# Kernel tuning notes

Hardware: AMD Instinct MI355X
Metric: run time of the kernel (lower is better)

The kernel has to match this reference:

```python
import jax, jax.numpy as jnp
import numpy as np

TOPK = 8
EPS = 1e-12  # matches torch F.normalize default eps


def setup_inputs() -> dict:
    key = jax.random.key(0)
    x = jax.random.normal(key, (8, 2048, 128), dtype=jnp.float32)
    return {"x": x}


def reference(x) -> jnp.ndarray:
    B, N, D = x.shape
    # --- pairwise dot scores on L2-normalized features (cosine similarity) ---
    norm = jnp.sqrt(jnp.sum(x * x, axis=-1, keepdims=True))
    normed = x / jnp.maximum(norm, EPS)
    scores = jnp.einsum('bnd,bmd->bnm', normed, normed)  # [B, N, N]

    # --- top-k per row -> binary adjacency via scatter ---
    _, idx = jax.lax.top_k(scores, TOPK)  # [B, N, k]
    bi = jnp.arange(B)[:, None, None]
    ni = jnp.arange(N)[None, :, None]
    adj = jnp.zeros((B, N, N), dtype=x.dtype).at[bi, ni, idx].set(1.0)

    # --- symmetrize and add self loops ---
    adj = jnp.maximum(adj, jnp.swapaxes(adj, 1, 2))
    eye = jnp.eye(N, dtype=x.dtype)
    adj = jnp.maximum(adj, eye[None, :, :])
    return adj
```

## Files before the change

kernel.cpp:

```cpp
#include <hip/hip_runtime.h>
#include <cstdint>

#define NN 2048
#define DD 128
#define BATCH 8
#define NROWS 16384
#define MARGIN 0.02f
#define CAP2 48

typedef __attribute__((ext_vector_type(8))) short bf16x8;
typedef __attribute__((ext_vector_type(4))) float f32x4;
typedef unsigned long long u64;
typedef unsigned int u32;
typedef unsigned short u16;

__device__ __forceinline__ u32 bf16rne(float f) {
  u32 u = __float_as_uint(f);
  return (u + 0x7fffu + ((u >> 16) & 1u)) >> 16;
}

__global__ __launch_bounds__(256) void k_normalize(const float* __restrict__ x,
                                                   double* __restrict__ rinv,
                                                   u32* __restrict__ nb,
                                                   float4* __restrict__ outz) {
  const int wave = threadIdx.x >> 6, lane = threadIdx.x & 63;
  const long long row = (long long)blockIdx.x * 4 + wave;
  float2 v = ((const float2*)(x + row * DD))[lane];
  const double d0 = v.x, d1 = v.y;
  double s = d0 * d0 + d1 * d1;
  #pragma unroll
  for (int m = 32; m >= 1; m >>= 1) s += __shfl_xor(s, m, 64);
  double den = sqrt(s); den = den > 1e-12 ? den : 1e-12;
  if (lane == 0) rinv[row] = 1.0 / den;
  double2 o; o.x = d0 / den; o.y = d1 / den;
  nb[row * (DD / 2) + lane] = bf16rne((float)o.x) | (bf16rne((float)o.y) << 16);

  {
    const int base = blockIdx.x * 256 + threadIdx.x;
    const float4 zf = {0.0f, 0.0f, 0.0f, 0.0f};
    #pragma unroll
    for (int k = 0; k < 8; ++k) outz[base + k * 1048576] = zf;
  }
}

#define CXF(i, j) { const float a_ = L[i], b_ = L[j]; L[i] = fmaxf(a_, b_); L[j] = fminf(a_, b_); }
__device__ __forceinline__ void merge8f(float (&kv)[8], const float (&ov)[8]) {
  float L[8];
  #pragma unroll
  for (int i = 0; i < 8; ++i) L[i] = fmaxf(kv[i], ov[7 - i]);
  CXF(0, 4) CXF(1, 5) CXF(2, 6) CXF(3, 7)
  CXF(0, 2) CXF(1, 3) CXF(4, 6) CXF(5, 7)
  CXF(0, 1) CXF(2, 3) CXF(4, 5) CXF(6, 7)
  #pragma unroll
  for (int i = 0; i < 8; ++i) kv[i] = L[i];
}

__device__ __forceinline__ u64 make_key(double s, int col) {
  u64 u = (u64)__double_as_longlong(s);
  const u64 m = (u64)((long long)u >> 63);
  u ^= (m | 0x8000000000000000ull);
  return (u & ~2047ull) | (u64)(2047 - col);
}
__device__ __forceinline__ u64 umax64(u64 a, u64 b) { return a > b ? a : b; }
__device__ __forceinline__ u64 umin64(u64 a, u64 b) { return a > b ? b : a; }
__device__ __forceinline__ void merge8(u64 (&kv)[8], const u64 (&ov)[8]) {
  u64 L[8];
  #pragma unroll
  for (int i = 0; i < 8; ++i) L[i] = umax64(kv[i], ov[7 - i]);
#define CX(i, j) { const u64 a_ = L[i], b_ = L[j]; L[i] = umax64(a_, b_); L[j] = umin64(a_, b_); }
  CX(0, 4) CX(1, 5) CX(2, 6) CX(3, 7)
  CX(0, 2) CX(1, 3) CX(4, 6) CX(5, 7)
  CX(0, 1) CX(2, 3) CX(4, 5) CX(6, 7)
#undef CX
  #pragma unroll
  for (int i = 0; i < 8; ++i) kv[i] = L[i];
}
__device__ __forceinline__ void insert8u(u64 (&v)[8], u64 nk) {
  if (nk > v[7]) {
    v[7] = nk;
    #pragma unroll
    for (int q = 7; q >= 1; --q) {
      const u64 a = v[q - 1], b = v[q];
      const bool sw = b > a;
      v[q - 1] = sw ? b : a; v[q] = sw ? a : b;
    }
  }
}

__global__ __launch_bounds__(1024) void k_build(const u32* __restrict__ nb,
                                                const float* __restrict__ x,
                                                const double* __restrict__ rinv,
                                                float* __restrict__ out) {
  __shared__ float bmf[64][130];
  __shared__ float thl[64];
  __shared__ u32 cnt[64];
  __shared__ u32 cand[64][CAP2];

  const int tid = threadIdx.x; const int w = tid >> 6; const int l = tid & 63;
  const int q = l >> 4; const int m = l & 15;
  const int rowblk = blockIdx.x;
  const int row0 = rowblk * 64;
  const int b = rowblk >> 5;
  const long long brow = (long long)b * NN;

  bf16x8 pvals = {0,0,0,0,0,0,0,0}, pones = {0,0,0,0,0,0,0,0};
  if (q == 0) {
    pvals[0] = (short)(__float_as_uint((float)(m + 1)) >> 16);
    pones[0] = (short)(__float_as_uint(1.0f) >> 16);
  }
  const f32x4 z4 = {0.0f, 0.0f, 0.0f, 0.0f};
  const f32x4 pr  = __builtin_amdgcn_mfma_f32_16x16x32_bf16(pvals, pones, z4, 0, 0, 0);
  const f32x4 pr2 = __builtin_amdgcn_mfma_f32_16x16x32_bf16(pones, pvals, z4, 0, 0, 0);
  int cof[4];
  #pragma unroll
  for (int p = 0; p < 4; ++p) cof[p] = (int)pr[p] - 1;
  const int rof = (int)pr2[0] - 1;

  if (tid < 64) cnt[tid] = 0u;

  bf16x8 ar4[4][4];
  #pragma unroll
  for (int rf = 0; rf < 4; ++rf) {
    const u32* Ap = nb + (long long)(row0 + 16 * rf + m) * (DD / 2) + 4 * q;
    #pragma unroll
    for (int cc = 0; cc < 4; ++cc) ar4[rf][cc] = *(const bf16x8*)(Ap + 16 * cc);
  }

  const int c0w = w * 128;
  const u32* Bb = nb + (brow + c0w) * (DD / 2);
  bf16x8 bcA[4], bcB[4];

#define LOADB(DST, T) { const u32* p_ = Bb + (long long)(16 * (T) + m) * (DD / 2) + 4 * q; \
  _Pragma("unroll") for (int cc = 0; cc < 4; ++cc) DST[cc] = *(const bf16x8*)(p_ + 16 * cc); }

#define TILE1(BC, T) {                                                             \
    _Pragma("unroll") for (int rf = 0; rf < 4; ++rf) {                             \
      f32x4 acc = z4;                                                              \
      _Pragma("unroll") for (int cc = 0; cc < 4; ++cc)                             \
        acc = __builtin_amdgcn_mfma_f32_16x16x32_bf16(BC[cc], ar4[rf][cc], acc, 0, 0, 0); \
      float bm_ = fmaxf(fmaxf(acc[0], acc[1]), fmaxf(acc[2], acc[3]));             \
      bm_ = fmaxf(bm_, __shfl_xor(bm_, 16, 64));                                   \
      bm_ = fmaxf(bm_, __shfl_xor(bm_, 32, 64));                                   \
      if (q == 0) bmf[16 * rf + m][w * 8 + (T)] = bm_;                             \
    } }

  LOADB(bcA, 0)
  #pragma unroll
  for (int t = 0; t < 8; t += 2) {
    LOADB(bcB, t + 1)
    TILE1(bcA, t)
    if (t + 2 < 8) LOADB(bcA, t + 2)
    TILE1(bcB, t + 1)
  }
#undef TILE1
  __syncthreads();

  for (int j = 0; j < 4; ++j) {
    const int rib = w * 4 + j;
    const float b0 = bmf[rib][2 * l];
    const float b1 = bmf[rib][2 * l + 1];
    float mx = fmaxf(b0, b1);
    float kv8[8];
    {
      const float o  = __shfl_xor(mx, 1, 64);
      const float h2 = fmaxf(mx, o), l2 = fminf(mx, o);
      const float p0 = __shfl_xor(h2, 2, 64), p1 = __shfl_xor(l2, 2, 64);
      const float m0 = fmaxf(h2, p0);
      const float xx = fminf(h2, p0);
      const float yy = fmaxf(l2, p1);
      const float m3 = fminf(l2, p1);
      const float m1 = fmaxf(xx, yy);
      const float m2 = fminf(xx, yy);
      const float q0 = __shfl_xor(m0, 4, 64), q1 = __shfl_xor(m1, 4, 64);
      const float q2 = __shfl_xor(m2, 4, 64), q3 = __shfl_xor(m3, 4, 64);
      float L[8] = {m0, m1, m2, m3, q3, q2, q1, q0};
      CXF(0, 4) CXF(1, 5) CXF(2, 6) CXF(3, 7)
      CXF(0, 2) CXF(1, 3) CXF(4, 6) CXF(5, 7)
      CXF(0, 1) CXF(2, 3) CXF(4, 5) CXF(6, 7)
      #pragma unroll
      for (int s = 0; s < 8; ++s) kv8[s] = L[s];
      #pragma unroll
      for (int mk = 8; mk <= 32; mk <<= 1) {
        float ov[8];
        #pragma unroll
        for (int s = 0; s < 8; ++s) ov[s] = __shfl_xor(kv8[s], mk, 64);
        merge8f(kv8, ov);
      }
    }
    if (l == 0) thl[rib] = kv8[7] - MARGIN;
  }
  __syncthreads();

  float th4[4]; int rib4[4];
  #pragma unroll
  for (int rf = 0; rf < 4; ++rf) {
    rib4[rf] = 16 * rf + rof;
    th4[rf] = thl[rib4[rf]];
  }

#define TILEF(BC, T) {                                                             \
    _Pragma("unroll") for (int rf = 0; rf < 4; ++rf) {                             \
      f32x4 acc = z4;                                                              \
      _Pragma("unroll") for (int cc = 0; cc < 4; ++cc)                             \
        acc = __builtin_amdgcn_mfma_f32_16x16x32_bf16(BC[cc], ar4[rf][cc], acc, 0, 0, 0); \
      _Pragma("unroll") for (int p = 0; p < 4; ++p) {                              \
        if (acc[p] >= th4[rf]) {                                                   \
          const u32 id = atomicAdd(&cnt[rib4[rf]], 1u);                            \
          if (id < CAP2) cand[rib4[rf]][id] = (u32)(c0w + 16 * (T) + cof[p]);      \
        }                                                                          \
      }                                                                            \
    } }

  LOADB(bcA, 0)
  #pragma unroll
  for (int t = 0; t < 8; t += 2) {
    LOADB(bcB, t + 1)
    TILEF(bcA, t)
    if (t + 2 < 8) LOADB(bcA, t + 2)
    TILEF(bcB, t + 1)
  }
#undef TILEF
#undef LOADB
  __syncthreads();

  for (int j = 0; j < 4; ++j) {
    const int rib = w * 4 + j;
    const int r = row0 + rib;
    const int n = r & (NN - 1);
    const int c = (int)cnt[rib];
    const double ri = rinv[r];
    u64 kv[8];
    #pragma unroll
    for (int s = 0; s < 8; ++s) kv[s] = 0ull;

    if (c <= CAP2) {
      float2 a4[4];
      #pragma unroll
      for (int jj = 0; jj < 4; ++jj)
        a4[jj] = ((const float2*)(x + (long long)r * DD))[m + 16 * jj];

      for (int i = 0; i < c; i += 4) {
        const int gi = i + q;
        const bool valid = gi < c;
        const int col = valid ? (int)cand[rib][gi] : 0;
        const float2* cp = (const float2*)(x + (brow + col) * DD);
        double d = 0.0;
        #pragma unroll
        for (int jj = 0; jj < 4; ++jj) {
          const float2 bv = cp[m + 16 * jj];
          d = fma((double)a4[jj].x, (double)bv.x, d);
          d = fma((double)a4[jj].y, (double)bv.y, d);
        }
        #pragma unroll
        for (int mk = 1; mk <= 8; mk <<= 1) d += __shfl_xor(d, mk, 64);
        if (valid) insert8u(kv, make_key(d * ri * rinv[brow + col], col));
      }
      #pragma unroll
      for (int mk = 16; mk <= 32; mk <<= 1) {
        u64 ov[8];
        #pragma unroll
        for (int s = 0; s < 8; ++s) ov[s] = __shfl_xor(kv[s], mk, 64);
        merge8(kv, ov);
      }
    } else {
      for (int base = 0; base < NN; base += 64) {
        const int col = base + l;
        const float* ap = x + (long long)r * DD;
        const float* cp2 = x + (brow + col) * DD;
        double d = 0.0;
        for (int kk = 0; kk < 64; ++kk) {
          const float2 av = ((const float2*)ap)[kk];
          const float2 bv = ((const float2*)cp2)[kk];
          d = fma((double)av.x, (double)bv.x, fma((double)av.y, (double)bv.y, d));
        }
        d = d * ri * rinv[brow + col];
        u64 one[8];
        one[0] = make_key(d, col);
        #pragma unroll
        for (int s = 1; s < 8; ++s) one[s] = 0ull;
        #pragma unroll
        for (int mk = 1; mk <= 32; mk <<= 1) {
          u64 ov[8];
          #pragma unroll
          for (int s = 0; s < 8; ++s) ov[s] = __shfl_xor(one[s], mk, 64);
          merge8(one, ov);
        }
        merge8(kv, one);
      }
    }

    const long long orow = (long long)r * NN;
    const long long obase = brow * NN;
    if (l == 8) out[orow + n] = 1.0f;
    #pragma unroll
    for (int s = 0; s < 8; ++s) {
      const int mcol = 2047 - (int)(kv[s] & 2047ull);
      if (l == s) {
        out[orow + mcol] = 1.0f;
        out[obase + (long long)mcol * NN + n] = 1.0f;
      }
    }
  }
}

extern "C" void kernel_launch(void* const* d_in, const int* in_sizes, int n_in,
                              void* d_out, int out_size, void* d_ws, size_t ws_size,
                              hipStream_t stream) {
  const float* x = (const float*)d_in[0];
  float* out = (float*)d_out;
  char* ws = (char*)d_ws;
  u32* nb = (u32*)ws;
  double* rinv = (double*)(ws + 4194304);

  hipLaunchKernelGGL(k_normalize, dim3(NROWS / 4), dim3(256), 0, stream, x, rinv, nb,
                     (float4*)out);
  hipLaunchKernelGGL(k_build, dim3(256), dim3(1024), 0, stream, nb, x, rinv, out);
}
```

Before: 228.6 us.

## Cache bf16-rounded scores in registers instead of recomputing the GEMM pass

The build kernel used to compute the score tiles twice: once to get per-tile maxima for a threshold, and again to collect candidates. It now runs a single MFMA pass and keeps the scores in registers, packed as bf16 values rounded upward so the threshold filter stays conservative. Blocks are retiled to 32 rows with 512 threads, each wave covering 256 columns, and the candidate capacity is raised to 64. This removes half of the MFMA work and the repeated B loads, at the cost of about 64 extra VGPRs per thread and possibly more candidates per row, since the rounded values are coarser.

Result: slower. 250.7 us (+9.7%).

```diff
diff --git a/kernel.cpp b/kernel.cpp
--- a/kernel.cpp
+++ b/kernel.cpp
@@ -6,7 +6,7 @@
 #define BATCH 8
 #define NROWS 16384
 #define MARGIN 0.02f
-#define CAP2 48
+#define CAP2 64
 
 typedef __attribute__((ext_vector_type(8))) short bf16x8;
 typedef __attribute__((ext_vector_type(4))) float f32x4;
@@ -17,6 +17,10 @@
 __device__ __forceinline__ u32 bf16rne(float f) {
   u32 u = __float_as_uint(f);
   return (u + 0x7fffu + ((u >> 16) & 1u)) >> 16;
+}
+__device__ __forceinline__ u32 bf16up(float f) {
+  const u32 u = __float_as_uint(f);
+  return (u + (((int)u >= 0) ? 0xFFFFu : 0u)) >> 16;
 }
 
 __global__ __launch_bounds__(256) void k_normalize(const float* __restrict__ x,
@@ -87,20 +91,19 @@
   }
 }
 
-__global__ __launch_bounds__(1024) void k_build(const u32* __restrict__ nb,
-                                                const float* __restrict__ x,
-                                                const double* __restrict__ rinv,
-                                                float* __restrict__ out) {
-  __shared__ float bmf[64][130];
-  __shared__ float thl[64];
-  __shared__ u32 cnt[64];
-  __shared__ u32 cand[64][CAP2];
+__global__ __launch_bounds__(512, 4) void k_build(const u32* __restrict__ nb,
+                                                  const float* __restrict__ x,
+                                                  const double* __restrict__ rinv,
+                                                  float* __restrict__ out) {
+  __shared__ float bmf[32][130];
+  __shared__ float thl[32];
+  __shared__ u32 cnt[32];
+  __shared__ u32 cand[32][CAP2];
 
   const int tid = threadIdx.x; const int w = tid >> 6; const int l = tid & 63;
   const int q = l >> 4; const int m = l & 15;
-  const int rowblk = blockIdx.x;
-  const int row0 = rowblk * 64;
-  const int b = rowblk >> 5;
+  const int row0 = blockIdx.x * 32;
+  const int b = blockIdx.x >> 6;
   const long long brow = (long long)b * NN;
 
   bf16x8 pvals = {0,0,0,0,0,0,0,0}, pones = {0,0,0,0,0,0,0,0};
@@ -116,43 +119,40 @@
   for (int p = 0; p < 4; ++p) cof[p] = (int)pr[p] - 1;
   const int rof = (int)pr2[0] - 1;
 
-  if (tid < 64) cnt[tid] = 0u;
-
-  bf16x8 ar4[4][4];
-  #pragma unroll
-  for (int rf = 0; rf < 4; ++rf) {
+  if (tid < 32) cnt[tid] = 0u;
+
+  bf16x8 ar4[2][4];
+  #pragma unroll
+  for (int rf = 0; rf < 2; ++rf) {
     const u32* Ap = nb + (long long)(row0 + 16 * rf + m) * (DD / 2) + 4 * q;
     #pragma unroll
     for (int cc = 0; cc < 4; ++cc) ar4[rf][cc] = *(const bf16x8*)(Ap + 16 * cc);
   }
 
-  const int c0w = w * 128;
+  const int c0w = w * 256;
   const u32* Bb = nb + (brow + c0w) * (DD / 2);
-  bf16x8 bcA[4], bcB[4];
-
-#define LOADB(DST, T) { const u32* p_ = Bb + (long long)(16 * (T) + m) * (DD / 2) + 4 * q; \
-  _Pragma("unroll") for (int cc = 0; cc < 4; ++cc) DST[cc] = *(const bf16x8*)(p_ + 16 * cc); }
-
-#define TILE1(BC, T) {                                                             \
-    _Pragma("unroll") for (int rf = 0; rf < 4; ++rf) {                             \
-      f32x4 acc = z4;                                                              \
-      _Pragma("unroll") for (int cc = 0; cc < 4; ++cc)                             \
-        acc = __builtin_amdgcn_mfma_f32_16x16x32_bf16(BC[cc], ar4[rf][cc], acc, 0, 0, 0); \
-      float bm_ = fmaxf(fmaxf(acc[0], acc[1]), fmaxf(acc[2], acc[3]));             \
-      bm_ = fmaxf(bm_, __shfl_xor(bm_, 16, 64));                                   \
-      bm_ = fmaxf(bm_, __shfl_xor(bm_, 32, 64));                                   \
-      if (q == 0) bmf[16 * rf + m][w * 8 + (T)] = bm_;                             \
-    } }
-
-  LOADB(bcA, 0)
-  #pragma unroll
-  for (int t = 0; t < 8; t += 2) {
-    LOADB(bcB, t + 1)
-    TILE1(bcA, t)
-    if (t + 2 < 8) LOADB(bcA, t + 2)
-    TILE1(bcB, t + 1)
-  }
-#undef TILE1
+  bf16x8 bc[4];
+  uint2 pk[32];
+
+  #pragma unroll
+  for (int t = 0; t < 16; ++t) {
+    { const u32* p_ = Bb + (long long)(16 * t + m) * (DD / 2) + 4 * q;
+      #pragma unroll
+      for (int cc = 0; cc < 4; ++cc) bc[cc] = *(const bf16x8*)(p_ + 16 * cc); }
+    #pragma unroll
+    for (int rf = 0; rf < 2; ++rf) {
+      f32x4 acc = z4;
+      #pragma unroll
+      for (int cc = 0; cc < 4; ++cc)
+        acc = __builtin_amdgcn_mfma_f32_16x16x32_bf16(bc[cc], ar4[rf][cc], acc, 0, 0, 0);
+      float bm_ = fmaxf(fmaxf(acc[0], acc[1]), fmaxf(acc[2], acc[3]));
+      bm_ = fmaxf(bm_, __shfl_xor(bm_, 16, 64));
+      bm_ = fmaxf(bm_, __shfl_xor(bm_, 32, 64));
+      if (q == 0) bmf[16 * rf + m][w * 16 + t] = bm_;
+      pk[t * 2 + rf].x = bf16up(acc[0]) | (bf16up(acc[1]) << 16);
+      pk[t * 2 + rf].y = bf16up(acc[2]) | (bf16up(acc[3]) << 16);
+    }
+  }
   __syncthreads();
 
   for (int j = 0; j < 4; ++j) {
@@ -191,36 +191,32 @@
   }
   __syncthreads();
 
-  float th4[4]; int rib4[4];
-  #pragma unroll
-  for (int rf = 0; rf < 4; ++rf) {
-    rib4[rf] = 16 * rf + rof;
-    th4[rf] = thl[rib4[rf]];
-  }
-
-#define TILEF(BC, T) {                                                             \
-    _Pragma("unroll") for (int rf = 0; rf < 4; ++rf) {                             \
-      f32x4 acc = z4;                                                              \
-      _Pragma("unroll") for (int cc = 0; cc < 4; ++cc)                             \
-        acc = __builtin_amdgcn_mfma_f32_16x16x32_bf16(BC[cc], ar4[rf][cc], acc, 0, 0, 0); \
-      _Pragma("unroll") for (int p = 0; p < 4; ++p) {                              \
-        if (acc[p] >= th4[rf]) {                                                   \
-          const u32 id = atomicAdd(&cnt[rib4[rf]], 1u);                            \
-          if (id < CAP2) cand[rib4[rf]][id] = (u32)(c0w + 16 * (T) + cof[p]);      \
-        }                                                                          \
-      }                                                                            \
-    } }
-
-  LOADB(bcA, 0)
-  #pragma unroll
-  for (int t = 0; t < 8; t += 2) {
-    LOADB(bcB, t + 1)
-    TILEF(bcA, t)
-    if (t + 2 < 8) LOADB(bcA, t + 2)
-    TILEF(bcB, t + 1)
-  }
-#undef TILEF
-#undef LOADB
+  {
+    float th2[2]; int rib2[2];
+    #pragma unroll
+    for (int rf = 0; rf < 2; ++rf) {
+      rib2[rf] = 16 * rf + rof;
+      th2[rf] = thl[rib2[rf]];
+    }
+    #pragma unroll
+    for (int t = 0; t < 16; ++t)
+      #pragma unroll
+      for (int rf = 0; rf < 2; ++rf) {
+        const uint2 pv = pk[t * 2 + rf];
+        float v0 = __uint_as_float(pv.x << 16);
+        float v1 = __uint_as_float(pv.x & 0xFFFF0000u);
+        float v2 = __uint_as_float(pv.y << 16);
+        float v3 = __uint_as_float(pv.y & 0xFFFF0000u);
+        #pragma unroll
+        for (int p = 0; p < 4; ++p) {
+          const float vv = (p == 0) ? v0 : (p == 1) ? v1 : (p == 2) ? v2 : v3;
+          if (vv >= th2[rf]) {
+            const u32 id = atomicAdd(&cnt[rib2[rf]], 1u);
+            if (id < CAP2) cand[rib2[rf]][id] = (u32)(c0w + 16 * t + cof[p]);
+          }
+        }
+      }
+  }
   __syncthreads();
 
   for (int j = 0; j < 4; ++j) {
@@ -314,5 +310,5 @@
 
   hipLaunchKernelGGL(k_normalize, dim3(NROWS / 4), dim3(256), 0, stream, x, rinv, nb,
                      (float4*)out);
-  hipLaunchKernelGGL(k_build, dim3(256), dim3(1024), 0, stream, nb, x, rinv, out);
-}
+  hipLaunchKernelGGL(k_build, dim3(512), dim3(512), 0, stream, nb, x, rinv, out);
+}
```
